# Kernel optimization log

Measured on AMD Instinct MI355X. Metric: run time of the kernel, lower is better.

## Reference

```python
import jax, jax.numpy as jnp
import numpy as np
import math

B, C, TC, H, W = 8, 256, 512, 48, 48
EPS = 1e-6

def setup_inputs() -> dict:
    key = jax.random.key(0)
    kx, kt, kq, kk, kv = jax.random.split(key, 5)
    x = jax.random.normal(kx, (B, C, H, W), dtype=jnp.float32)
    token = jax.random.normal(kt, (B, TC, H, W), dtype=jnp.float32)
    # xavier_uniform for 1x1 conv weights [out, in]
    def xavier(k, fan_out, fan_in):
        a = math.sqrt(6.0 / (fan_in + fan_out))
        return jax.random.uniform(k, (fan_out, fan_in), dtype=jnp.float32, minval=-a, maxval=a)
    Wq = xavier(kq, C, C)
    Wk = xavier(kk, C, TC)
    Wv = xavier(kv, C, TC)
    alpha = jnp.float32(0.5)  # nonzero so the attention path affects the output
    return {"x": x, "token": token, "Wq": Wq, "Wk": Wk, "Wv": Wv, "alpha": alpha}

def reference(x, token, Wq, Wk, Wv, alpha):
    # 1x1 convs == per-pixel GEMMs over the channel dim
    q = jnp.einsum('oc,bchw->bohw', Wq, x)       # [B,C,H,W]
    k = jnp.einsum('oc,bchw->bohw', Wk, token)   # [B,C,H,W]
    v = jnp.einsum('oc,bchw->bohw', Wv, token)   # [B,C,H,W]
    b, c, h, w = q.shape
    n = h * w
    qf = q.reshape(b, c, n).transpose(0, 2, 1)   # [B,N,C]
    kf = k.reshape(b, c, n)                      # [B,C,N]
    vf = v.reshape(b, c, n).transpose(0, 2, 1)   # [B,N,C]
    # cosine normalization over the channel dim (F.normalize with eps clamp)
    qn = qf / jnp.maximum(jnp.linalg.norm(qf, axis=-1, keepdims=True), EPS)
    kn = kf / jnp.maximum(jnp.linalg.norm(kf, axis=1, keepdims=True), EPS)
    attn = jnp.einsum('bnc,bcm->bnm', qn, kn) / math.sqrt(c)  # [B,N,N]
    attn = jax.nn.softmax(attn, axis=-1)
    out = jnp.einsum('bnm,bmc->bnc', attn, vf)   # [B,N,C]
    out = out.transpose(0, 2, 1).reshape(b, c, h, w)
    return x + alpha * out
```

## Files before the change

### kernel.cpp

```cpp
#include <hip/hip_runtime.h>

#define B_   8
#define C_   256
#define TC_  512
#define HW_  2304
#define EPS_ 1e-6f

typedef __bf16 bf16_t;
typedef __bf16 bf16x8 __attribute__((ext_vector_type(8)));
typedef __bf16 bf16x4_t __attribute__((ext_vector_type(4)));
typedef float  f32x4 __attribute__((ext_vector_type(4)));
typedef unsigned int  u32;
typedef unsigned int  u32x2 __attribute__((ext_vector_type(2)));
typedef unsigned int  u32x4 __attribute__((ext_vector_type(4)));
typedef long long     i64;
typedef unsigned char u8;

__device__ __forceinline__ void g2l16(const void* g, void* l) {
    __builtin_amdgcn_global_load_lds(
        (const __attribute__((address_space(1))) unsigned int*)g,
        (__attribute__((address_space(3))) unsigned int*)l, 16, 0, 0);
}

__device__ __forceinline__ u8 to_fp8(float v) {
    return (u8)(__builtin_amdgcn_cvt_pk_fp8_f32(v, v, 0, false) & 0xff);
}

__global__ __launch_bounds__(256)
void wfrag_kernel(const float* __restrict__ wq, const float* __restrict__ wk,
                  const float* __restrict__ wv,
                  bf16_t* __restrict__ oq, bf16_t* __restrict__ ok,
                  bf16_t* __restrict__ ov)
{
    const int fid = blockIdx.x * 4 + (threadIdx.x >> 6);
    const int lane = threadIdx.x & 63;
    const int l16 = lane & 15, quad = lane >> 4;

    const float* src; bf16_t* dst; int cin, f;
    if (fid < 128)      { src = wq; dst = oq; cin = C_;  f = fid; }
    else if (fid < 384) { src = wk; dst = ok; cin = TC_; f = fid - 128; }
    else                { src = wv; dst = ov; cin = TC_; f = fid - 384; }
    const int nks = cin / 32;
    const int ot = f / nks, ks = f % nks;

    const float* s = src + (size_t)(ot * 16 + l16) * cin + ks * 32 + quad * 8;
    float4 a = *(const float4*)(s);
    float4 b = *(const float4*)(s + 4);
    bf16x8 o;
    o[0] = (__bf16)a.x; o[1] = (__bf16)a.y; o[2] = (__bf16)a.z; o[3] = (__bf16)a.w;
    o[4] = (__bf16)b.x; o[5] = (__bf16)b.y; o[6] = (__bf16)b.z; o[7] = (__bf16)b.w;
    *(bf16x8*)(dst + (size_t)f * 512 + lane * 8) = o;
}

template<int CIN, bool DO_V>
__global__ __launch_bounds__(256, 4)
void convqkv_kernel(const float* __restrict__ X, const bf16_t* __restrict__ Wa,
                    const bf16_t* __restrict__ Wvp, u8* __restrict__ outA,
                    u8* __restrict__ outV)
{
    const int bid = blockIdx.x;
    const int b  = bid & 7;
    const int n0 = (bid >> 3) * 16;
    const int tid = threadIdx.x;
    const int wv = tid >> 6;
    const int lane = tid & 63;
    const int quad = lane >> 4, l16 = lane & 15;
    const int NKS = CIN / 32;

    __shared__ bf16_t T[16][CIN + 8];
    __shared__ float ssp[4][16];

    {
        const float* Xb = X + (size_t)b * CIN * HW_ + n0;
        const int cl = tid >> 2;
        const int n4 = (tid & 3) * 4;
#pragma unroll
        for (int cp = 0; cp < CIN; cp += 64) {
            float4 v = *(const float4*)(Xb + (size_t)(cp + cl) * HW_ + n4);
            T[n4 + 0][cp + cl] = (__bf16)v.x;
            T[n4 + 1][cp + cl] = (__bf16)v.y;
            T[n4 + 2][cp + cl] = (__bf16)v.z;
            T[n4 + 3][cp + cl] = (__bf16)v.w;
        }
    }
    __syncthreads();

    bf16x8 af[CIN / 32];
#pragma unroll
    for (int ks = 0; ks < CIN / 32; ks++)
        af[ks] = *(const bf16x8*)(&T[l16][ks * 32 + quad * 8]);

    const int ot0 = wv * 4;

    f32x4 accK[4];
#pragma unroll
    for (int p = 0; p < 4; p++) accK[p] = (f32x4){0.f, 0.f, 0.f, 0.f};
    {
        const bf16_t* wbase = Wa + ((size_t)ot0 * NKS) * 512 + lane * 8;
#pragma unroll
        for (int ks = 0; ks < CIN / 32; ks++)
#pragma unroll
            for (int p = 0; p < 4; p++) {
                bf16x8 bw = *(const bf16x8*)(wbase + (size_t)(p * NKS + ks) * 512);
                accK[p] = __builtin_amdgcn_mfma_f32_16x16x32_bf16(af[ks], bw, accK[p], 0, 0, 0);
            }
    }

    {
        float ssr[4];
#pragma unroll
        for (int r = 0; r < 4; r++) {
            float ss = accK[0][r] * accK[0][r] + accK[1][r] * accK[1][r]
                     + accK[2][r] * accK[2][r] + accK[3][r] * accK[3][r];
            ss += __shfl_xor(ss, 1);
            ss += __shfl_xor(ss, 2);
            ss += __shfl_xor(ss, 4);
            ss += __shfl_xor(ss, 8);
            ssr[r] = ss;
        }
        if (l16 == 0) {
#pragma unroll
            for (int r = 0; r < 4; r++) ssp[wv][quad * 4 + r] = ssr[r];
        }
    }

    f32x4 accV[4];
    if (DO_V) {
#pragma unroll
        for (int p = 0; p < 4; p++) accV[p] = (f32x4){0.f, 0.f, 0.f, 0.f};
        const bf16_t* wbase = Wvp + ((size_t)ot0 * NKS) * 512 + lane * 8;
#pragma unroll
        for (int ks = 0; ks < CIN / 32; ks++)
#pragma unroll
            for (int p = 0; p < 4; p++) {
                bf16x8 aw = *(const bf16x8*)(wbase + (size_t)(p * NKS + ks) * 512);
                accV[p] = __builtin_amdgcn_mfma_f32_16x16x32_bf16(aw, af[ks], accV[p], 0, 0, 0);
            }
    }

    __syncthreads();

    float scale[4];
#pragma unroll
    for (int r = 0; r < 4; r++) {
        int px = quad * 4 + r;
        float s = ssp[0][px] + ssp[1][px] + ssp[2][px] + ssp[3][px];
        scale[r] = 1.0f / fmaxf(sqrtf(s), EPS_);
    }
    {
        u8* oa = outA + ((size_t)b * HW_ + n0 + quad * 4) * C_ + l16;
#pragma unroll
        for (int p = 0; p < 4; p++)
#pragma unroll
            for (int r = 0; r < 4; r++)
                oa[(size_t)r * C_ + (ot0 + p) * 16] = to_fp8(accK[p][r] * scale[r]);
    }

    if (DO_V) {
#pragma unroll
        for (int p = 0; p < 4; p++)
#pragma unroll
            for (int r = 0; r < 4; r++)
                outV[((size_t)b * C_ + (ot0 + p) * 16 + quad * 4 + r) * HW_ + n0 + l16]
                    = to_fp8(accV[p][r]);
    }
}

__global__ __launch_bounds__(256, 4)
void attn_part_kernel(const u8* __restrict__ q8, const u8* __restrict__ k8,
                      const u8* __restrict__ v8,
                      bf16_t* __restrict__ Opart, float* __restrict__ lpart,
                      int tilesPerSplit, int JS)
{
    const int bid = blockIdx.x;
    const int b   = bid & 7;
    const int rr  = bid >> 3;
    const int js  = rr % JS;
    const int mt  = rr / JS;
    const int wv   = threadIdx.x >> 6;
    const int lane = threadIdx.x & 63;
    const int quad = lane >> 4;
    const int l16  = lane & 15;
    const int row0 = mt * 64 + wv * 16;
    const int jbase = js * tilesPerSplit * 32;

    const u8* qb = q8 + (size_t)b * HW_ * C_;
    const u8* kb = k8 + (size_t)b * HW_ * C_;
    const u8* vb = v8 + (size_t)b * C_ * HW_;

    __shared__ u8 Kbuf[2][8192];
    __shared__ u8 Vbuf[2][8192];
    __shared__ u8 Pt[4][896];

    i64 aq[8];
    {
        const u8* r0 = qb + (size_t)(row0 + l16) * C_ + quad * 8;
#pragma unroll
        for (int t = 0; t < 8; t++) aq[t] = *(const i64*)(r0 + t * 32);
    }

    f32x4 O[16];
#pragma unroll
    for (int i = 0; i < 16; i++) O[i] = (f32x4){0.f, 0.f, 0.f, 0.f};
    float lsum[4] = {0.f, 0.f, 0.f, 0.f};

    const int kj = lane & 31;
    const int kh = lane >> 5;
    const int vg = (lane & 1) ^ ((lane >> 3) & 1);
    const int vc = lane >> 1;

#define STAGE(bufi, j0g)                                                       \
    {                                                                          \
        _Pragma("unroll")                                                      \
        for (int p = 0; p < 2; p++) {                                          \
            int i = wv * 2 + p;                                                \
            int s = i * 2 + kh;                                                \
            g2l16(kb + (size_t)((j0g) + kj) * C_ + s * 16,                     \
                  &Kbuf[bufi][i * 1024]);                                      \
        }                                                                      \
        _Pragma("unroll")                                                      \
        for (int p = 0; p < 2; p++) {                                          \
            int i = wv * 2 + p;                                                \
            int c = i * 32 + vc;                                               \
            g2l16(vb + (size_t)c * HW_ + (j0g) + vg * 16,                      \
                  &Vbuf[bufi][i * 1024]);                                      \
        }                                                                      \
    }

    STAGE(0, jbase)

    u8* pw = &Pt[wv][0];
    const int koff  = (quad >> 1) * 512 + l16 * 16 + (quad & 1) * 8;
    const int vbase = l16 * 32 + ((((quad >> 1) ^ (l16 >> 2)) & 1) << 4)
                    + (quad & 1) * 8;
    const u32 sel = (quad < 2) ? 0x06040200u : 0x07050301u;

    for (int tt = 0; tt < tilesPerSplit; tt++) {
        __syncthreads();
        if (tt + 1 < tilesPerSplit) STAGE((tt + 1) & 1, jbase + (tt + 1) * 32)

        const u8* Kb = Kbuf[tt & 1];
        const u8* Vb = Vbuf[tt & 1];

        f32x4 s00 = (f32x4){0.f,0.f,0.f,0.f}, s01 = (f32x4){0.f,0.f,0.f,0.f};
#pragma unroll
        for (int t = 0; t < 8; t++) {
            i64 bk0 = *(const i64*)(Kb + t * 1024 + koff);
            i64 bk1 = *(const i64*)(Kb + t * 1024 + koff + 256);
            s00 = __builtin_amdgcn_mfma_f32_16x16x32_fp8_fp8(aq[t], bk0, s00, 0, 0, 0);
            s01 = __builtin_amdgcn_mfma_f32_16x16x32_fp8_fp8(aq[t], bk1, s01, 0, 0, 0);
        }
#pragma unroll
        for (int r = 0; r < 4; r++) {
            float p00 = __expf(s00[r] * 0.0625f), p01 = __expf(s01[r] * 0.0625f);
            lsum[r] += p00 + p01;
            u32 w0 = __builtin_amdgcn_cvt_pk_fp8_f32(p00, p01, 0, false);
            *(short*)(pw + (quad * 4 + r) * 56 + l16 * 2) = (short)w0;
        }
        i64 ap0;
        {
            const u8* pr = pw + l16 * 56 + (quad & 1) * 16;
            u32x2 dA = *(const u32x2*)(pr);
            u32x2 dB = *(const u32x2*)(pr + 8);
            u32 lo = __builtin_amdgcn_perm(dA[1], dA[0], sel);
            u32 hi = __builtin_amdgcn_perm(dB[1], dB[0], sel);
            ap0 = ((i64)hi << 32) | (i64)lo;
        }
#pragma unroll
        for (int ct = 0; ct < 16; ct++) {
            i64 bv = *(const i64*)(Vb + ct * 512 + vbase);
            O[ct] = __builtin_amdgcn_mfma_f32_16x16x32_fp8_fp8(ap0, bv, O[ct], 0, 0, 0);
        }
    }

#pragma unroll
    for (int r = 0; r < 4; r++) {
        float t0 = lsum[r];
        t0 += __shfl_xor(t0, 1); t0 += __shfl_xor(t0, 2);
        t0 += __shfl_xor(t0, 4); t0 += __shfl_xor(t0, 8);
        lsum[r] = t0;
    }
    float* lp = lpart + (size_t)(js * B_ + b) * HW_;
    if (l16 == 0) {
        float4 a0; a0.x = lsum[0]; a0.y = lsum[1]; a0.z = lsum[2]; a0.w = lsum[3];
        *(float4*)(lp + row0 + quad * 4) = a0;
    }
    bf16_t* op = Opart + (size_t)(js * B_ + b) * C_ * HW_;
#pragma unroll
    for (int ct = 0; ct < 16; ct++) {
        int c = ct * 16 + l16;
        bf16x4_t v0;
        v0[0] = (__bf16)O[ct][0]; v0[1] = (__bf16)O[ct][1];
        v0[2] = (__bf16)O[ct][2]; v0[3] = (__bf16)O[ct][3];
        *(bf16x4_t*)(op + (size_t)c * HW_ + row0 + quad * 4) = v0;
    }
#undef STAGE
}

__global__ __launch_bounds__(256)
void epilogue_kernel(const float* __restrict__ x, const bf16_t* __restrict__ Opart,
                     const float* __restrict__ lpart, const float* __restrict__ alphaPtr,
                     float* __restrict__ out, int JS)
{
    const float a = *alphaPtr;
    const size_t S = (size_t)B_ * C_ * HW_;
    size_t flat = ((size_t)blockIdx.x * 256 + threadIdx.x) * 4;
    int bc = (int)(flat / HW_);
    int n  = (int)(flat % HW_);
    int b  = bc >> 8;
    float4 xv = *(const float4*)(x + flat);
    float s0 = 0.f, s1 = 0.f, s2 = 0.f, s3 = 0.f;
    float l0 = 0.f, l1 = 0.f, l2 = 0.f, l3 = 0.f;
    for (int js = 0; js < JS; js++) {
        bf16x4_t ov = *(const bf16x4_t*)(Opart + (size_t)js * S + flat);
        s0 += (float)ov[0]; s1 += (float)ov[1];
        s2 += (float)ov[2]; s3 += (float)ov[3];
        float4 lv = *(const float4*)(lpart + (size_t)(js * B_ + b) * HW_ + n);
        l0 += lv.x; l1 += lv.y; l2 += lv.z; l3 += lv.w;
    }
    float4 r;
    r.x = xv.x + a * s0 / l0;
    r.y = xv.y + a * s1 / l1;
    r.z = xv.z + a * s2 / l2;
    r.w = xv.w + a * s3 / l3;
    *(float4*)(out + flat) = r;
}

extern "C" void kernel_launch(void* const* d_in, const int* in_sizes, int n_in,
                              void* d_out, int out_size, void* d_ws, size_t ws_size,
                              hipStream_t stream)
{
    (void)in_sizes; (void)n_in; (void)out_size;
    const float* x     = (const float*)d_in[0];
    const float* token = (const float*)d_in[1];
    const float* Wq    = (const float*)d_in[2];
    const float* Wk    = (const float*)d_in[3];
    const float* Wv    = (const float*)d_in[4];
    const float* alpha = (const float*)d_in[5];
    float* out = (float*)d_out;

    const size_t S = (size_t)B_ * HW_ * C_;

    int JS = 8;
    for (;;) {
        size_t need = (12 + 2 * (size_t)JS) * S
                    + (size_t)JS * B_ * HW_ * 4 + (size_t)B_ * HW_ * 4;
        if (need <= ws_size || JS == 1) break;
        JS >>= 1;
    }
    const int tilesPerSplit = (HW_ / 32) / JS;

    char* ws = (char*)d_ws;
    bf16_t* WqL   = (bf16_t*)(ws + 6 * S);
    bf16_t* WkL   = WqL + (size_t)C_ * C_;
    bf16_t* WvL   = WkL + (size_t)C_ * TC_;
    u8*     q8    = (u8*)(ws + 7 * S);
    u8*     k8    = (u8*)(ws + 8 * S);
    u8*     v8    = (u8*)(ws + 9 * S);
    bf16_t* Opart = (bf16_t*)(ws + 12 * S);
    float*  lpart = (float*)(ws + (12 + 2 * (size_t)JS) * S);

    wfrag_kernel<<<dim3(160), dim3(256), 0, stream>>>(Wq, Wk, Wv, WqL, WkL, WvL);
    convqkv_kernel<C_,  false><<<dim3(B_ * HW_ / 16), dim3(256), 0, stream>>>(x,     WqL, nullptr, q8, nullptr);
    convqkv_kernel<TC_, true ><<<dim3(B_ * HW_ / 16), dim3(256), 0, stream>>>(token, WkL, WvL,     k8, v8);
    attn_part_kernel<<<dim3(JS * B_ * (HW_ / 64)), dim3(256), 0, stream>>>(q8, k8, v8, Opart, lpart, tilesPerSplit, JS);
    epilogue_kernel<<<dim3((int)(S / 1024)), dim3(256), 0, stream>>>(x, Opart, lpart, alpha, out, JS);
}
```

Before: 236.7 us.

## Transpose score MFMA and reshuffle P via permlane swaps instead of LDS

The QK^T MFMA operands are swapped so each lane holds a column of scores, and the exp'd probabilities are packed to fp8 and moved into the A-operand layout for the PV MFMA with v_permlane32/16_swap rather than a write/read round trip through a per-wave LDS scratch buffer. Row sums become a single scalar per lane reduced with two shuffles. The key-split count drops from 8 to 4, halving the partial outputs written and merged but giving fewer blocks. Correctness depends on the permlane swap sequence producing exactly the operand layout the PV MFMA expects.

```diff
diff --git a/kernel.cpp b/kernel.cpp
--- a/kernel.cpp
+++ b/kernel.cpp
@@ -11,8 +11,6 @@
 typedef __bf16 bf16x4_t __attribute__((ext_vector_type(4)));
 typedef float  f32x4 __attribute__((ext_vector_type(4)));
 typedef unsigned int  u32;
-typedef unsigned int  u32x2 __attribute__((ext_vector_type(2)));
-typedef unsigned int  u32x4 __attribute__((ext_vector_type(4)));
 typedef long long     i64;
 typedef unsigned char u8;
 
@@ -190,7 +188,6 @@
 
     __shared__ u8 Kbuf[2][8192];
     __shared__ u8 Vbuf[2][8192];
-    __shared__ u8 Pt[4][896];
 
     i64 aq[8];
     {
@@ -202,7 +199,7 @@
     f32x4 O[16];
 #pragma unroll
     for (int i = 0; i < 16; i++) O[i] = (f32x4){0.f, 0.f, 0.f, 0.f};
-    float lsum[4] = {0.f, 0.f, 0.f, 0.f};
+    float lsum = 0.f;
 
     const int kj = lane & 31;
     const int kh = lane >> 5;
@@ -229,11 +226,9 @@
 
     STAGE(0, jbase)
 
-    u8* pw = &Pt[wv][0];
     const int koff  = (quad >> 1) * 512 + l16 * 16 + (quad & 1) * 8;
     const int vbase = l16 * 32 + ((((quad >> 1) ^ (l16 >> 2)) & 1) << 4)
                     + (quad & 1) * 8;
-    const u32 sel = (quad < 2) ? 0x06040200u : 0x07050301u;
 
     for (int tt = 0; tt < tilesPerSplit; tt++) {
         __syncthreads();
@@ -247,25 +242,25 @@
         for (int t = 0; t < 8; t++) {
             i64 bk0 = *(const i64*)(Kb + t * 1024 + koff);
             i64 bk1 = *(const i64*)(Kb + t * 1024 + koff + 256);
-            s00 = __builtin_amdgcn_mfma_f32_16x16x32_fp8_fp8(aq[t], bk0, s00, 0, 0, 0);
-            s01 = __builtin_amdgcn_mfma_f32_16x16x32_fp8_fp8(aq[t], bk1, s01, 0, 0, 0);
-        }
-#pragma unroll
-        for (int r = 0; r < 4; r++) {
-            float p00 = __expf(s00[r] * 0.0625f), p01 = __expf(s01[r] * 0.0625f);
-            lsum[r] += p00 + p01;
-            u32 w0 = __builtin_amdgcn_cvt_pk_fp8_f32(p00, p01, 0, false);
-            *(short*)(pw + (quad * 4 + r) * 56 + l16 * 2) = (short)w0;
-        }
-        i64 ap0;
-        {
-            const u8* pr = pw + l16 * 56 + (quad & 1) * 16;
-            u32x2 dA = *(const u32x2*)(pr);
-            u32x2 dB = *(const u32x2*)(pr + 8);
-            u32 lo = __builtin_amdgcn_perm(dA[1], dA[0], sel);
-            u32 hi = __builtin_amdgcn_perm(dB[1], dB[0], sel);
-            ap0 = ((i64)hi << 32) | (i64)lo;
-        }
+            s00 = __builtin_amdgcn_mfma_f32_16x16x32_fp8_fp8(bk0, aq[t], s00, 0, 0, 0);
+            s01 = __builtin_amdgcn_mfma_f32_16x16x32_fp8_fp8(bk1, aq[t], s01, 0, 0, 0);
+        }
+
+        float pA0 = __expf(s00[0] * 0.0625f), pA1 = __expf(s00[1] * 0.0625f);
+        float pA2 = __expf(s00[2] * 0.0625f), pA3 = __expf(s00[3] * 0.0625f);
+        float pB0 = __expf(s01[0] * 0.0625f), pB1 = __expf(s01[1] * 0.0625f);
+        float pB2 = __expf(s01[2] * 0.0625f), pB3 = __expf(s01[3] * 0.0625f);
+        lsum += (pA0 + pA1 + pA2 + pA3) + (pB0 + pB1 + pB2 + pB3);
+
+        u32 A = __builtin_amdgcn_cvt_pk_fp8_f32(pA0, pA1, 0, false);
+        A     = __builtin_amdgcn_cvt_pk_fp8_f32(pA2, pA3, A, true);
+        u32 Bw = __builtin_amdgcn_cvt_pk_fp8_f32(pB0, pB1, 0, false);
+        Bw     = __builtin_amdgcn_cvt_pk_fp8_f32(pB2, pB3, Bw, true);
+
+        asm volatile("v_permlane32_swap_b32 %0, %1" : "+v"(A), "+v"(Bw));
+        asm volatile("v_permlane16_swap_b32 %0, %1" : "+v"(A), "+v"(Bw));
+        i64 ap0 = ((i64)(u32)Bw << 32) | (i64)A;
+
 #pragma unroll
         for (int ct = 0; ct < 16; ct++) {
             i64 bv = *(const i64*)(Vb + ct * 512 + vbase);
@@ -273,18 +268,11 @@
         }
     }
 
-#pragma unroll
-    for (int r = 0; r < 4; r++) {
-        float t0 = lsum[r];
-        t0 += __shfl_xor(t0, 1); t0 += __shfl_xor(t0, 2);
-        t0 += __shfl_xor(t0, 4); t0 += __shfl_xor(t0, 8);
-        lsum[r] = t0;
-    }
+    lsum += __shfl_xor(lsum, 16);
+    lsum += __shfl_xor(lsum, 32);
     float* lp = lpart + (size_t)(js * B_ + b) * HW_;
-    if (l16 == 0) {
-        float4 a0; a0.x = lsum[0]; a0.y = lsum[1]; a0.z = lsum[2]; a0.w = lsum[3];
-        *(float4*)(lp + row0 + quad * 4) = a0;
-    }
+    if (quad == 0) lp[row0 + l16] = lsum;
+
     bf16_t* op = Opart + (size_t)(js * B_ + b) * C_ * HW_;
 #pragma unroll
     for (int ct = 0; ct < 16; ct++) {
@@ -341,7 +329,7 @@
 
     const size_t S = (size_t)B_ * HW_ * C_;
 
-    int JS = 8;
+    int JS = 4;
     for (;;) {
         size_t need = (12 + 2 * (size_t)JS) * S
                     + (size_t)JS * B_ * HW_ * 4 + (size_t)B_ * HW_ * 4;
```

New measurement: 222.6 us. 6.0% less time.
